# Kernel optimization log

Hardware: AMD Instinct MI355X
Metric: run time of the kernel (lower is better)

The kernel has to match this reference:

```python
import jax, jax.numpy as jnp
import numpy as np

NEG = -65504.0
D = 640


def _linear(x, W, b):
    return x @ W + b


def _qkv_attention(q, k, v, mask4):
    # q:[B,Lq,D] k,v:[B,Lk,D] mask4:[B,1,1,Lk] (True = masked)
    scores = jnp.einsum('bqd,bkd->bqk', q, k) / jnp.sqrt(jnp.asarray(q.shape[-1], q.dtype))
    scores = jnp.where(mask4[:, 0, :, :], NEG, scores)  # mask.squeeze(1) -> [B,1,Lk]
    p = jax.nn.softmax(scores, axis=-1)
    return jnp.einsum('bqk,bkd->bqd', p, v)


def _attflat(x, mask4, W1, b1, W2, b2, Wm, bm):
    # x:[B,N,D]; glimpses == 1
    att = _linear(jax.nn.relu(_linear(x, W1, b1)), W2, b2)  # [B,N,1]
    m = mask4[:, 0, 0, :, None]                              # [B,N,1]
    att = jnp.where(m, NEG, att)
    att = jax.nn.softmax(att, axis=1)
    pooled = jnp.sum(att * x, axis=1)                        # [B,D]
    return _linear(pooled, Wm, bm), att[..., 0]              # att.squeeze() -> [B,N]


def setup_inputs() -> dict:
    key = jax.random.key(0)
    ks = jax.random.split(key, 16)
    B, Ni, Nq = 64, 512, 128
    s = 0.02
    inp = {
        'i_batch': jax.random.normal(ks[0], (B, Ni, D), jnp.float32),
        'q_batch': jax.random.normal(ks[1], (B, Nq, D), jnp.float32),
        'i_mask': jax.random.bernoulli(ks[2], 0.3, (B, 1, 1, Ni)),
        'q_mask': jax.random.bernoulli(ks[3], 0.3, (B, 1, 1, Nq)),
        # l_flatten params (applied to image-side features)
        'lW1': jax.random.normal(ks[4], (D, 2 * D), jnp.float32) * s,
        'lb1': jnp.zeros((2 * D,), jnp.float32),
        'lW2': jax.random.normal(ks[5], (2 * D, 1), jnp.float32) * s,
        'lb2': jnp.zeros((1,), jnp.float32),
        'lWm': jax.random.normal(ks[6], (D, D), jnp.float32) * s,
        'lbm': jnp.zeros((D,), jnp.float32),
        # i_flatten params (applied to language-side features)
        'iW1': jax.random.normal(ks[7], (D, 2 * D), jnp.float32) * s,
        'ib1': jnp.zeros((2 * D,), jnp.float32),
        'iW2': jax.random.normal(ks[8], (2 * D, 1), jnp.float32) * s,
        'ib2': jnp.zeros((1,), jnp.float32),
        'iWm': jax.random.normal(ks[9], (D, D), jnp.float32) * s,
        'ibm': jnp.zeros((D,), jnp.float32),
    }
    return inp


def reference(i_batch, q_batch, i_mask, q_mask,
              lW1, lb1, lW2, lb2, lWm, lbm,
              iW1, ib1, iW2, ib2, iWm, ibm):
    # image attends over question tokens
    i_feat = _qkv_attention(i_batch, q_batch, q_batch, q_mask)   # [B,Ni,D]
    i_feat, i_weight = _attflat(i_feat, i_mask, lW1, lb1, lW2, lb2, lWm, lbm)
    # question attends over image regions
    l_feat = _qkv_attention(q_batch, i_batch, i_batch, i_mask)   # [B,Nq,D]
    l_feat, _ = _attflat(l_feat, q_mask, iW1, ib1, iW2, ib2, iWm, ibm)
    return (i_feat, l_feat, i_weight)
```

## Files before the change

kernel.cpp:

```cpp
#include <hip/hip_runtime.h>
#include <cstdint>

#define DEV __device__ __forceinline__

typedef __attribute__((ext_vector_type(8))) short bf16x8;
typedef __attribute__((ext_vector_type(4))) float f32x4;

static constexpr int B  = 64;
static constexpr int NI = 512;
static constexpr int NQ = 128;
static constexpr int D  = 640;
static constexpr int H  = 1280;
static constexpr float NEGV  = -65504.0f;
static constexpr float SCALE = 0.039528470752104745f;

DEV unsigned short f2bf(float f) {
  union { float f; uint32_t u; } c; c.f = f;
  uint32_t u = c.u;
  u += 0x7fffu + ((u >> 16) & 1u);
  return (unsigned short)(u >> 16);
}
DEV float bf2f(unsigned short h) {
  union { uint32_t u; float f; } c; c.u = ((uint32_t)h) << 16;
  return c.f;
}

DEV int xcd_swz(int bid, int nwg) {
  return (bid & 7) * (nwg >> 3) + (bid >> 3);
}

DEV void gll16(const void* g, void* l) {
  __builtin_amdgcn_global_load_lds(
      (const __attribute__((address_space(1))) void*)(uintptr_t)g,
      (__attribute__((address_space(3))) void*)(uint32_t)(uintptr_t)l,
      16, 0, 0);
}

DEV void stage64(const unsigned short* src, int ld, unsigned short* lds, int tid) {
  const int w = tid >> 6, lane = tid & 63;
#pragma unroll
  for (int i = 0; i < 4; ++i) {
    int c = w * 256 + i * 64 + lane;
    int r = c >> 3, ck = c & 7;
    int col8 = ((ck ^ (r & 7)) << 3);
    gll16(src + (long)r * ld + col8, (char*)lds + (size_t)c * 16);
  }
}

DEV bf16x8 frag(const unsigned short* ls, int row, int q) {
  return *(const bf16x8*)&ls[row * 64 + (((q ^ (row & 7))) << 3)];
}

template<int OUT_BF16>
__global__ __launch_bounds__(256, 4) void gemm_nt(
    const unsigned short* __restrict__ A, const unsigned short* __restrict__ Bt,
    void* __restrict__ C, int lda, int ldb, int ldc, int K,
    long sA, long sB, long sC, int gx, int gy)
{
  __shared__ __align__(16) unsigned short lsA[128 * 64];
  __shared__ __align__(16) unsigned short lsB[128 * 64];
  const int tid = threadIdx.x;
  const int w = tid >> 6, lane = tid & 63;
  const int wm = w >> 1, wn = w & 1;
  const int g = lane >> 4, r = lane & 15;
  const int wg = xcd_swz(blockIdx.x, gridDim.x);
  const int bz = wg / (gx * gy);
  const int r2 = wg - bz * gx * gy;
  const int by = r2 / gx;
  const int bx = r2 - by * gx;
  const long zb = bz;
  const unsigned short* Ab = A + zb * sA + (long)bx * 128 * lda;
  const unsigned short* Bb = Bt + zb * sB + (long)by * 128 * ldb;

  f32x4 acc[4][4] = {};
  for (int k0 = 0; k0 < K; k0 += 64) {
    stage64(Ab + k0, lda, lsA, tid);
    stage64(Bb + k0, ldb, lsB, tid);
    __syncthreads();
#pragma unroll
    for (int kk = 0; kk < 2; ++kk) {
      bf16x8 af[4], bfr[4];
#pragma unroll
      for (int mi = 0; mi < 4; ++mi) af[mi]  = frag(lsA, wm * 64 + mi * 16 + r, kk * 4 + g);
#pragma unroll
      for (int ni = 0; ni < 4; ++ni) bfr[ni] = frag(lsB, wn * 64 + ni * 16 + r, kk * 4 + g);
#pragma unroll
      for (int mi = 0; mi < 4; ++mi)
#pragma unroll
        for (int ni = 0; ni < 4; ++ni)
          acc[mi][ni] = __builtin_amdgcn_mfma_f32_16x16x32_bf16(af[mi], bfr[ni], acc[mi][ni], 0, 0, 0);
    }
    __syncthreads();
  }
  const int row0 = bx * 128 + wm * 64;
  const int col0 = by * 128 + wn * 64;
#pragma unroll
  for (int mi = 0; mi < 4; ++mi)
#pragma unroll
    for (int ni = 0; ni < 4; ++ni)
#pragma unroll
      for (int j = 0; j < 4; ++j) {
        int rr = row0 + mi * 16 + g * 4 + j;
        int cc = col0 + ni * 16 + r;
        float v = acc[mi][ni][j];
        if (OUT_BF16)
          ((unsigned short*)C)[zb * sC + (long)rr * ldc + cc] = f2bf(v);
        else
          ((float*)C)[zb * sC + (long)rr * ldc + cc] = v;
      }
}

__global__ __launch_bounds__(256, 2) void qksm_k(
    const unsigned short* __restrict__ A, const unsigned short* __restrict__ Bt,
    const int* __restrict__ mask, unsigned short* __restrict__ P)
{
  __shared__ __align__(16) float S[128 * 128];
  unsigned short* lsA = (unsigned short*)S;
  unsigned short* lsB = lsA + 128 * 64;
  const int tid = threadIdx.x;
  const int w = tid >> 6, lane = tid & 63;
  const int wm = w >> 1, wn = w & 1;
  const int g = lane >> 4, r = lane & 15;
  const int wg = xcd_swz(blockIdx.x, gridDim.x);
  const int mt = wg & 3, b = wg >> 2;
  const unsigned short* Ab = A + ((long)b * NI + (long)mt * 128) * D;
  const unsigned short* Bb = Bt + (long)b * NQ * D;

  f32x4 acc[4][4] = {};
  for (int k0 = 0; k0 < D; k0 += 64) {
    stage64(Ab + k0, D, lsA, tid);
    stage64(Bb + k0, D, lsB, tid);
    __syncthreads();
#pragma unroll
    for (int kk = 0; kk < 2; ++kk) {
      bf16x8 af[4], bfr[4];
#pragma unroll
      for (int mi = 0; mi < 4; ++mi) af[mi]  = frag(lsA, wm * 64 + mi * 16 + r, kk * 4 + g);
#pragma unroll
      for (int ni = 0; ni < 4; ++ni) bfr[ni] = frag(lsB, wn * 64 + ni * 16 + r, kk * 4 + g);
#pragma unroll
      for (int mi = 0; mi < 4; ++mi)
#pragma unroll
        for (int ni = 0; ni < 4; ++ni)
          acc[mi][ni] = __builtin_amdgcn_mfma_f32_16x16x32_bf16(af[mi], bfr[ni], acc[mi][ni], 0, 0, 0);
    }
    __syncthreads();
  }
#pragma unroll
  for (int mi = 0; mi < 4; ++mi)
#pragma unroll
    for (int ni = 0; ni < 4; ++ni)
#pragma unroll
      for (int j = 0; j < 4; ++j) {
        int rr = wm * 64 + mi * 16 + g * 4 + j;
        int cc = wn * 64 + ni * 16 + r;
        S[rr * 128 + (cc ^ ((rr & 7) << 2))] = acc[mi][ni][j] * SCALE;
      }
  __syncthreads();
  const int* mk = mask + (long)b * NQ;
  const int mk0 = mk[lane], mk1 = mk[lane + 64];
  for (int t = 0; t < 32; ++t) {
    const int rr = w * 32 + t;
    const int off = (rr & 7) << 2;
    float x0 = mk0 ? NEGV : S[rr * 128 + (lane ^ off)];
    float x1 = mk1 ? NEGV : S[rr * 128 + ((lane + 64) ^ off)];
    float mx = fmaxf(x0, x1);
#pragma unroll
    for (int s = 32; s >= 1; s >>= 1) mx = fmaxf(mx, __shfl_xor(mx, s));
    float e0 = __expf(x0 - mx), e1 = __expf(x1 - mx);
    float sum = e0 + e1;
#pragma unroll
    for (int s = 32; s >= 1; s >>= 1) sum += __shfl_xor(sum, s);
    const float inv = 1.f / sum;
    unsigned short* pr = P + ((long)b * NI + (long)mt * 128 + rr) * NQ;
    pr[lane] = f2bf(e0 * inv);
    pr[lane + 64] = f2bf(e1 * inv);
  }
}

__global__ __launch_bounds__(256, 4) void hatt_k(
    const unsigned short* __restrict__ A, const unsigned short* __restrict__ Bt,
    const float* __restrict__ b1, const float* __restrict__ W2,
    float* __restrict__ outlogit)
{
  constexpr int NH = H / 128;
  __shared__ __align__(16) unsigned short lsA[128 * 64];
  __shared__ __align__(16) unsigned short lsB[128 * 64];
  __shared__ float b1c[128], w2c[128];
  const int tid = threadIdx.x;
  const int w = tid >> 6, lane = tid & 63;
  const int wm = w >> 1, wn = w & 1;
  const int g = lane >> 4, r = lane & 15;
  const int wg = xcd_swz(blockIdx.x, gridDim.x);
  const int n0 = (wg % NH) * 128;
  const int m0 = (wg / NH) * 128;
  if (tid < 128) { b1c[tid] = b1[n0 + tid]; w2c[tid] = W2[n0 + tid]; }
  const unsigned short* Ab = A + (long)m0 * D;
  const unsigned short* Bb = Bt + (long)n0 * D;

  f32x4 acc[4][4] = {};
  for (int k0 = 0; k0 < D; k0 += 64) {
    stage64(Ab + k0, D, lsA, tid);
    stage64(Bb + k0, D, lsB, tid);
    __syncthreads();
#pragma unroll
    for (int kk = 0; kk < 2; ++kk) {
      bf16x8 af[4], bfr[4];
#pragma unroll
      for (int mi = 0; mi < 4; ++mi) af[mi]  = frag(lsA, wm * 64 + mi * 16 + r, kk * 4 + g);
#pragma unroll
      for (int ni = 0; ni < 4; ++ni) bfr[ni] = frag(lsB, wn * 64 + ni * 16 + r, kk * 4 + g);
#pragma unroll
      for (int mi = 0; mi < 4; ++mi)
#pragma unroll
        for (int ni = 0; ni < 4; ++ni)
          acc[mi][ni] = __builtin_amdgcn_mfma_f32_16x16x32_bf16(af[mi], bfr[ni], acc[mi][ni], 0, 0, 0);
    }
    __syncthreads();
  }
  float rs[4][4];
#pragma unroll
  for (int mi = 0; mi < 4; ++mi)
#pragma unroll
    for (int j = 0; j < 4; ++j) rs[mi][j] = 0.f;
#pragma unroll
  for (int mi = 0; mi < 4; ++mi)
#pragma unroll
    for (int ni = 0; ni < 4; ++ni)
#pragma unroll
      for (int j = 0; j < 4; ++j) {
        int cl = wn * 64 + ni * 16 + r;
        float h = acc[mi][ni][j] + b1c[cl];
        h = fmaxf(h, 0.f);
        rs[mi][j] += h * w2c[cl];
      }
#pragma unroll
  for (int mi = 0; mi < 4; ++mi)
#pragma unroll
    for (int j = 0; j < 4; ++j) {
      float v = rs[mi][j];
      v += __shfl_xor(v, 1); v += __shfl_xor(v, 2);
      v += __shfl_xor(v, 4); v += __shfl_xor(v, 8);
      if (r == 0) atomicAdd(&outlogit[m0 + wm * 64 + mi * 16 + g * 4 + j], v);
    }
}

template<int L>
__global__ void sm_scores(const float* __restrict__ S, const int* __restrict__ mask,
                          unsigned short* __restrict__ P, int M)
{
  constexpr int NV = L / 64;
  const int wid = threadIdx.x >> 6, lane = threadIdx.x & 63;
  const long row = (long)blockIdx.x * 4 + wid;
  const int b = (int)(row / M);
  const float* s = S + row * (long)L;
  const int* mk = mask + (long)b * L;
  float x[NV];
  float mx = -__builtin_inff();
#pragma unroll
  for (int i = 0; i < NV; ++i) {
    int idx = i * 64 + lane;
    float v = s[idx] * SCALE;
    x[i] = mk[idx] ? NEGV : v;
    mx = fmaxf(mx, x[i]);
  }
#pragma unroll
  for (int sft = 32; sft >= 1; sft >>= 1) mx = fmaxf(mx, __shfl_xor(mx, sft));
  float sum = 0.f;
#pragma unroll
  for (int i = 0; i < NV; ++i) { x[i] = __expf(x[i] - mx); sum += x[i]; }
#pragma unroll
  for (int sft = 32; sft >= 1; sft >>= 1) sum += __shfl_xor(sum, sft);
  const float inv = 1.f / sum;
  unsigned short* p = P + row * (long)L;
#pragma unroll
  for (int i = 0; i < NV; ++i) p[i * 64 + lane] = f2bf(x[i] * inv);
}

template<int L>
__global__ void sm_att(const float* __restrict__ logit, const int* __restrict__ mask,
                       const float* __restrict__ b2p, float* __restrict__ att,
                       float* __restrict__ iw)
{
  constexpr int PER = (L + 255) / 256;
  __shared__ float red[4];
  const int tid = threadIdx.x, b = blockIdx.x;
  const float b2v = b2p[0];
  float xs[PER];
  float mx = -__builtin_inff();
#pragma unroll
  for (int i = 0; i < PER; ++i) {
    int idx = tid + i * 256;
    if (idx < L) {
      float v = mask[(long)b * L + idx] ? NEGV : (logit[(long)b * L + idx] + b2v);
      xs[i] = v; mx = fmaxf(mx, v);
    } else xs[i] = -__builtin_inff();
  }
#pragma unroll
  for (int s = 32; s >= 1; s >>= 1) mx = fmaxf(mx, __shfl_xor(mx, s));
  if ((tid & 63) == 0) red[tid >> 6] = mx;
  __syncthreads();
  mx = fmaxf(fmaxf(red[0], red[1]), fmaxf(red[2], red[3]));
  __syncthreads();
  float sum = 0.f;
#pragma unroll
  for (int i = 0; i < PER; ++i) {
    int idx = tid + i * 256;
    if (idx < L) { xs[i] = __expf(xs[i] - mx); sum += xs[i]; }
  }
#pragma unroll
  for (int s = 32; s >= 1; s >>= 1) sum += __shfl_xor(sum, s);
  if ((tid & 63) == 0) red[tid >> 6] = sum;
  __syncthreads();
  sum = red[0] + red[1] + red[2] + red[3];
  const float inv = 1.f / sum;
#pragma unroll
  for (int i = 0; i < PER; ++i) {
    int idx = tid + i * 256;
    if (idx < L) {
      float a = xs[i] * inv;
      att[(long)b * L + idx] = a;
      if (iw) iw[(long)b * L + idx] = a;
    }
  }
}

template<int L>
__global__ void pooled_k(const float* __restrict__ att, const unsigned short* __restrict__ X,
                         float* __restrict__ out)
{
  __shared__ float a[L];
  __shared__ float2 part[8][64];
  const int b = blockIdx.x, tid = threadIdx.x;
  const int lane = tid & 63, grp = tid >> 6;
  const int d0 = blockIdx.y * 128 + lane * 2;
  for (int i = tid; i < L; i += 512) a[i] = att[(long)b * L + i];
  __syncthreads();
  const unsigned short* xb = X + (long)b * L * D + d0;
  float s0 = 0.f, s1 = 0.f;
  const int m0 = grp * (L / 8);
#pragma unroll 4
  for (int m = m0; m < m0 + L / 8; ++m) {
    ushort2 v = *(const ushort2*)&xb[(long)m * D];
    float av = a[m];
    s0 += av * bf2f(v.x); s1 += av * bf2f(v.y);
  }
  part[grp][lane] = make_float2(s0, s1);
  __syncthreads();
  if (tid < 64) {
    float r0 = 0.f, r1 = 0.f;
#pragma unroll
    for (int gi = 0; gi < 8; ++gi) { r0 += part[gi][tid].x; r1 += part[gi][tid].y; }
    *(float2*)&out[b * D + blockIdx.y * 128 + tid * 2] = make_float2(r0, r1);
  }
}

__global__ void final_k(const float* __restrict__ pooled, const float* __restrict__ W,
                        const float* __restrict__ bias, float* __restrict__ out)
{
  __shared__ float p[160];
  const int b = blockIdx.x, tid = threadIdx.x;
  const int nn = blockIdx.y * 128 + tid;
  const int k0 = blockIdx.z * 160;
  for (int i = tid; i < 160; i += 128) p[i] = pooled[b * D + k0 + i];
  __syncthreads();
  float acc = (blockIdx.z == 0) ? bias[nn] : 0.f;
  for (int k = 0; k < 160; ++k) acc += p[k] * W[(long)(k0 + k) * D + nn];
  atomicAdd(&out[b * D + nn], acc);
}

template<int WRITE_N>
__global__ void cast_t_k(const float* __restrict__ in, unsigned short* __restrict__ outN,
                         unsigned short* __restrict__ outT, int R, int C)
{
  __shared__ float t[64][65];
  const int tid = threadIdx.x;
  const int cg = tid & 15, rw = tid >> 4;
  const long base = (long)blockIdx.z * R * C;
  const int c0 = blockIdx.x * 64, r0 = blockIdx.y * 64;
#pragma unroll
  for (int p = 0; p < 4; ++p) {
    int row = p * 16 + rw;
    float4 v = *(const float4*)&in[base + (long)(r0 + row) * C + c0 + cg * 4];
    *(float4*)&t[row][cg * 4] = v;
    if (WRITE_N) {
      ushort4 o;
      o.x = f2bf(v.x); o.y = f2bf(v.y); o.z = f2bf(v.z); o.w = f2bf(v.w);
      *(ushort4*)&outN[base + (long)(r0 + row) * C + c0 + cg * 4] = o;
    }
  }
  __syncthreads();
#pragma unroll
  for (int p = 0; p < 4; ++p) {
    int ocol = p * 16 + rw;
    ushort4 o;
    o.x = f2bf(t[cg * 4 + 0][ocol]);
    o.y = f2bf(t[cg * 4 + 1][ocol]);
    o.z = f2bf(t[cg * 4 + 2][ocol]);
    o.w = f2bf(t[cg * 4 + 3][ocol]);
    *(ushort4*)&outT[base + (long)(c0 + ocol) * R + r0 + cg * 4] = o;
  }
}

extern "C" void kernel_launch(void* const* d_in, const int* in_sizes, int n_in,
                              void* d_out, int out_size, void* d_ws, size_t ws_size,
                              hipStream_t stream)
{
  (void)in_sizes; (void)n_in; (void)out_size; (void)ws_size;
  const float* i_batch = (const float*)d_in[0];
  const float* q_batch = (const float*)d_in[1];
  const int*   i_mask  = (const int*)d_in[2];
  const int*   q_mask  = (const int*)d_in[3];
  const float* lW1 = (const float*)d_in[4];
  const float* lb1 = (const float*)d_in[5];
  const float* lW2 = (const float*)d_in[6];
  const float* lb2 = (const float*)d_in[7];
  const float* lWm = (const float*)d_in[8];
  const float* lbm = (const float*)d_in[9];
  const float* iW1 = (const float*)d_in[10];
  const float* ib1 = (const float*)d_in[11];
  const float* iW2 = (const float*)d_in[12];
  const float* ib2 = (const float*)d_in[13];
  const float* iWm = (const float*)d_in[14];
  const float* ibm = (const float*)d_in[15];
  float* out_if = (float*)d_out;
  float* out_lf = out_if + B * D;
  float* out_iw = out_lf + B * D;

  char* wp = (char*)d_ws;
  size_t off = 0;
  auto alloc = [&](size_t bytes) { void* p = wp + off; off += (bytes + 255) & ~(size_t)255; return p; };
  unsigned short* i_bf   = (unsigned short*)alloc((size_t)B * NI * D * 2);
  unsigned short* i_bfT  = (unsigned short*)alloc((size_t)B * NI * D * 2);
  unsigned short* q_bf   = (unsigned short*)alloc((size_t)B * NQ * D * 2);
  unsigned short* q_bfT  = (unsigned short*)alloc((size_t)B * NQ * D * 2);
  unsigned short* x1_bf  = (unsigned short*)alloc((size_t)B * NI * D * 2);
  unsigned short* x2_bf  = (unsigned short*)alloc((size_t)B * NQ * D * 2);
  float*          scores = (float*)alloc((size_t)B * NQ * NI * 4);
  unsigned short* p_bf   = (unsigned short*)alloc((size_t)B * NI * NQ * 2);
  unsigned short* lW1t   = (unsigned short*)alloc((size_t)H * D * 2);
  unsigned short* iW1t   = (unsigned short*)alloc((size_t)H * D * 2);
  float* logit1  = (float*)alloc((size_t)B * NI * 4);
  float* att1    = (float*)alloc((size_t)B * NI * 4);
  float* logit2  = (float*)alloc((size_t)B * NQ * 4);
  float* att2    = (float*)alloc((size_t)B * NQ * 4);
  float* pooled1 = (float*)alloc((size_t)B * D * 4);
  float* pooled2 = (float*)alloc((size_t)B * D * 4);

  hipMemsetAsync(out_if, 0, (size_t)2 * B * D * 4, stream);
  hipMemsetAsync(logit1, 0, (size_t)(B * NI * 2 + B * NQ * 2) * 4, stream);

  cast_t_k<1><<<dim3(D / 64, NI / 64, B), 256, 0, stream>>>(i_batch, i_bf, i_bfT, NI, D);
  cast_t_k<1><<<dim3(D / 64, NQ / 64, B), 256, 0, stream>>>(q_batch, q_bf, q_bfT, NQ, D);
  cast_t_k<0><<<dim3(H / 64, D / 64, 1), 256, 0, stream>>>(lW1, nullptr, lW1t, D, H);
  cast_t_k<0><<<dim3(H / 64, D / 64, 1), 256, 0, stream>>>(iW1, nullptr, iW1t, D, H);

  qksm_k<<<dim3(4 * B), 256, 0, stream>>>(i_bf, q_bf, q_mask, p_bf);
  gemm_nt<1><<<dim3((NI / 128) * (D / 128) * B), 256, 0, stream>>>(
      p_bf, q_bfT, x1_bf, NQ, NQ, D, NQ, (long)NI * NQ, (long)D * NQ, (long)NI * D,
      NI / 128, D / 128);
  hatt_k<<<dim3((H / 128) * (B * NI / 128)), 256, 0, stream>>>(x1_bf, lW1t, lb1, lW2, logit1);
  sm_att<NI><<<dim3(B), 256, 0, stream>>>(logit1, i_mask, lb2, att1, out_iw);
  pooled_k<NI><<<dim3(B, D / 128), 512, 0, stream>>>(att1, x1_bf, pooled1);
  final_k<<<dim3(B, D / 128, 4), 128, 0, stream>>>(pooled1, lWm, lbm, out_if);

  gemm_nt<0><<<dim3((NQ / 128) * (NI / 128) * B), 256, 0, stream>>>(
      q_bf, i_bf, scores, D, D, NI, D, (long)NQ * D, (long)NI * D, (long)NQ * NI,
      NQ / 128, NI / 128);
  sm_scores<NI><<<dim3(B * NQ / 4), 256, 0, stream>>>(scores, i_mask, p_bf, NQ);
  gemm_nt<1><<<dim3((NQ / 128) * (D / 128) * B), 256, 0, stream>>>(
      p_bf, i_bfT, x2_bf, NI, NI, D, NI, (long)NQ * NI, (long)D * NI, (long)NQ * D,
      NQ / 128, D / 128);
  hatt_k<<<dim3((H / 128) * (B * NQ / 128)), 256, 0, stream>>>(x2_bf, iW1t, ib1, iW2, logit2);
  sm_att<NQ><<<dim3(B), 256, 0, stream>>>(logit2, q_mask, ib2, att2, nullptr);
  pooled_k<NQ><<<dim3(B, D / 128), 512, 0, stream>>>(att2, x2_bf, pooled2);
  final_k<<<dim3(B, D / 128, 4), 128, 0, stream>>>(pooled2, iWm, ibm, out_lf);
}
```

Baseline: 427.8 us.

## Fuse first attention into flash-style kernel, double-buffer GEMMs, fuse attflat tail

Replaces the first QK^T+softmax kernel and the following PV GEMM with one fused kernel. It keeps the probability tile in LDS and multiplies it by the transposed V in chunks, so the P matrix never goes to global memory. The generic GEMM and hatt kernels now double-buffer their LDS tiles, which overlaps the next tile's load with the current MFMA work but halves the occupancy bound. The softmax, pooling and final linear kernels are merged into a single per-batch tail kernel, which removes memsets and atomics but runs only 64 blocks with serial loops.

```diff
diff --git a/kernel.cpp b/kernel.cpp
--- a/kernel.cpp
+++ b/kernel.cpp
@@ -36,11 +36,12 @@
       16, 0, 0);
 }
 
-DEV void stage64(const unsigned short* src, int ld, unsigned short* lds, int tid) {
+template<int ROWS>
+DEV void stageT(const unsigned short* src, int ld, unsigned short* lds, int tid) {
   const int w = tid >> 6, lane = tid & 63;
 #pragma unroll
-  for (int i = 0; i < 4; ++i) {
-    int c = w * 256 + i * 64 + lane;
+  for (int i = 0; i < ROWS / 32; ++i) {
+    int c = w * (ROWS * 2) + i * 64 + lane;
     int r = c >> 3, ck = c & 7;
     int col8 = ((ck ^ (r & 7)) << 3);
     gll16(src + (long)r * ld + col8, (char*)lds + (size_t)c * 16);
@@ -48,17 +49,20 @@
 }
 
 DEV bf16x8 frag(const unsigned short* ls, int row, int q) {
-  return *(const bf16x8*)&ls[row * 64 + (((q ^ (row & 7))) << 3)];
+  return *(const bf16x8*)&ls[row * 64 + ((q ^ (row & 7)) << 3)];
+}
+DEV bf16x8 fragP(const unsigned short* P, int row, int q) {
+  return *(const bf16x8*)&P[row * 128 + ((q ^ (row & 7)) << 3)];
 }
 
 template<int OUT_BF16>
-__global__ __launch_bounds__(256, 4) void gemm_nt(
+__global__ __launch_bounds__(256, 2) void gemm_nt(
     const unsigned short* __restrict__ A, const unsigned short* __restrict__ Bt,
     void* __restrict__ C, int lda, int ldb, int ldc, int K,
     long sA, long sB, long sC, int gx, int gy)
 {
-  __shared__ __align__(16) unsigned short lsA[128 * 64];
-  __shared__ __align__(16) unsigned short lsB[128 * 64];
+  __shared__ __align__(16) unsigned short lsA[2][128 * 64];
+  __shared__ __align__(16) unsigned short lsB[2][128 * 64];
   const int tid = threadIdx.x;
   const int w = tid >> 6, lane = tid & 63;
   const int wm = w >> 1, wn = w & 1;
@@ -72,25 +76,31 @@
   const unsigned short* Ab = A + zb * sA + (long)bx * 128 * lda;
   const unsigned short* Bb = Bt + zb * sB + (long)by * 128 * ldb;
 
+  const int nt = K >> 6;
+  stageT<128>(Ab, lda, lsA[0], tid);
+  stageT<128>(Bb, ldb, lsB[0], tid);
   f32x4 acc[4][4] = {};
-  for (int k0 = 0; k0 < K; k0 += 64) {
-    stage64(Ab + k0, lda, lsA, tid);
-    stage64(Bb + k0, ldb, lsB, tid);
+  for (int t = 0; t < nt; ++t) {
     __syncthreads();
+    if (t + 1 < nt) {
+      stageT<128>(Ab + (t + 1) * 64, lda, lsA[(t + 1) & 1], tid);
+      stageT<128>(Bb + (t + 1) * 64, ldb, lsB[(t + 1) & 1], tid);
+    }
+    const unsigned short* la = lsA[t & 1];
+    const unsigned short* lb = lsB[t & 1];
 #pragma unroll
     for (int kk = 0; kk < 2; ++kk) {
       bf16x8 af[4], bfr[4];
 #pragma unroll
-      for (int mi = 0; mi < 4; ++mi) af[mi]  = frag(lsA, wm * 64 + mi * 16 + r, kk * 4 + g);
-#pragma unroll
-      for (int ni = 0; ni < 4; ++ni) bfr[ni] = frag(lsB, wn * 64 + ni * 16 + r, kk * 4 + g);
+      for (int mi = 0; mi < 4; ++mi) af[mi]  = frag(la, wm * 64 + mi * 16 + r, kk * 4 + g);
+#pragma unroll
+      for (int ni = 0; ni < 4; ++ni) bfr[ni] = frag(lb, wn * 64 + ni * 16 + r, kk * 4 + g);
 #pragma unroll
       for (int mi = 0; mi < 4; ++mi)
 #pragma unroll
         for (int ni = 0; ni < 4; ++ni)
           acc[mi][ni] = __builtin_amdgcn_mfma_f32_16x16x32_bf16(af[mi], bfr[ni], acc[mi][ni], 0, 0, 0);
     }
-    __syncthreads();
   }
   const int row0 = bx * 128 + wm * 64;
   const int col0 = by * 128 + wn * 64;
@@ -110,82 +120,175 @@
       }
 }
 
-__global__ __launch_bounds__(256, 2) void qksm_k(
-    const unsigned short* __restrict__ A, const unsigned short* __restrict__ Bt,
-    const int* __restrict__ mask, unsigned short* __restrict__ P)
-{
-  __shared__ __align__(16) float S[128 * 128];
-  unsigned short* lsA = (unsigned short*)S;
-  unsigned short* lsB = lsA + 128 * 64;
+__global__ __launch_bounds__(256, 2) void fattn1_k(
+    const unsigned short* __restrict__ Qm,
+    const unsigned short* __restrict__ Km,
+    const unsigned short* __restrict__ Vt,
+    const int* __restrict__ mask,
+    unsigned short* __restrict__ O)
+{
+  __shared__ __align__(16) unsigned short sh[64 * 64 + 128 * 64];
+  __shared__ __align__(16) unsigned short lsV[2][128 * 64];
+  __shared__ float red0[64][2], red1[64][2];
+  unsigned short* lsQ = sh;
+  unsigned short* lsK = sh + 64 * 64;
+  unsigned short* Pl  = sh;
   const int tid = threadIdx.x;
   const int w = tid >> 6, lane = tid & 63;
   const int wm = w >> 1, wn = w & 1;
   const int g = lane >> 4, r = lane & 15;
   const int wg = xcd_swz(blockIdx.x, gridDim.x);
-  const int mt = wg & 3, b = wg >> 2;
-  const unsigned short* Ab = A + ((long)b * NI + (long)mt * 128) * D;
-  const unsigned short* Bb = Bt + (long)b * NQ * D;
-
-  f32x4 acc[4][4] = {};
+  const int mt = wg & 7, b = wg >> 3;
+  const unsigned short* Qb = Qm + ((long)b * NI + (long)mt * 64) * D;
+  const unsigned short* Kb = Km + (long)b * NQ * D;
+  const unsigned short* Vb = Vt + (long)b * D * NQ;
+
+  int mki[4];
+#pragma unroll
+  for (int ni = 0; ni < 4; ++ni) mki[ni] = mask[b * NQ + wn * 64 + ni * 16 + r];
+
+  f32x4 acc[2][4] = {};
   for (int k0 = 0; k0 < D; k0 += 64) {
-    stage64(Ab + k0, D, lsA, tid);
-    stage64(Bb + k0, D, lsB, tid);
+    stageT<64>(Qb + k0, D, lsQ, tid);
+    stageT<128>(Kb + k0, D, lsK, tid);
     __syncthreads();
 #pragma unroll
     for (int kk = 0; kk < 2; ++kk) {
-      bf16x8 af[4], bfr[4];
-#pragma unroll
-      for (int mi = 0; mi < 4; ++mi) af[mi]  = frag(lsA, wm * 64 + mi * 16 + r, kk * 4 + g);
-#pragma unroll
-      for (int ni = 0; ni < 4; ++ni) bfr[ni] = frag(lsB, wn * 64 + ni * 16 + r, kk * 4 + g);
-#pragma unroll
-      for (int mi = 0; mi < 4; ++mi)
+      bf16x8 af[2], bfr[4];
+#pragma unroll
+      for (int mi = 0; mi < 2; ++mi) af[mi]  = frag(lsQ, wm * 32 + mi * 16 + r, kk * 4 + g);
+#pragma unroll
+      for (int ni = 0; ni < 4; ++ni) bfr[ni] = frag(lsK, wn * 64 + ni * 16 + r, kk * 4 + g);
+#pragma unroll
+      for (int mi = 0; mi < 2; ++mi)
 #pragma unroll
         for (int ni = 0; ni < 4; ++ni)
           acc[mi][ni] = __builtin_amdgcn_mfma_f32_16x16x32_bf16(af[mi], bfr[ni], acc[mi][ni], 0, 0, 0);
     }
     __syncthreads();
   }
-#pragma unroll
-  for (int mi = 0; mi < 4; ++mi)
+
+  float x[2][4][4], pm[2][4];
+#pragma unroll
+  for (int mi = 0; mi < 2; ++mi)
+#pragma unroll
+    for (int j = 0; j < 4; ++j) pm[mi][j] = -3.4e38f;
+#pragma unroll
+  for (int mi = 0; mi < 2; ++mi)
 #pragma unroll
     for (int ni = 0; ni < 4; ++ni)
 #pragma unroll
       for (int j = 0; j < 4; ++j) {
-        int rr = wm * 64 + mi * 16 + g * 4 + j;
-        int cc = wn * 64 + ni * 16 + r;
-        S[rr * 128 + (cc ^ ((rr & 7) << 2))] = acc[mi][ni][j] * SCALE;
+        float v = mki[ni] ? NEGV : acc[mi][ni][j] * SCALE;
+        x[mi][ni][j] = v;
+        pm[mi][j] = fmaxf(pm[mi][j], v);
       }
-  __syncthreads();
-  const int* mk = mask + (long)b * NQ;
-  const int mk0 = mk[lane], mk1 = mk[lane + 64];
-  for (int t = 0; t < 32; ++t) {
-    const int rr = w * 32 + t;
-    const int off = (rr & 7) << 2;
-    float x0 = mk0 ? NEGV : S[rr * 128 + (lane ^ off)];
-    float x1 = mk1 ? NEGV : S[rr * 128 + ((lane + 64) ^ off)];
-    float mx = fmaxf(x0, x1);
-#pragma unroll
-    for (int s = 32; s >= 1; s >>= 1) mx = fmaxf(mx, __shfl_xor(mx, s));
-    float e0 = __expf(x0 - mx), e1 = __expf(x1 - mx);
-    float sum = e0 + e1;
-#pragma unroll
-    for (int s = 32; s >= 1; s >>= 1) sum += __shfl_xor(sum, s);
-    const float inv = 1.f / sum;
-    unsigned short* pr = P + ((long)b * NI + (long)mt * 128 + rr) * NQ;
-    pr[lane] = f2bf(e0 * inv);
-    pr[lane + 64] = f2bf(e1 * inv);
-  }
-}
-
-__global__ __launch_bounds__(256, 4) void hatt_k(
+#pragma unroll
+  for (int s = 1; s < 16; s <<= 1)
+#pragma unroll
+    for (int mi = 0; mi < 2; ++mi)
+#pragma unroll
+      for (int j = 0; j < 4; ++j) pm[mi][j] = fmaxf(pm[mi][j], __shfl_xor(pm[mi][j], s));
+  if (r == 0) {
+#pragma unroll
+    for (int mi = 0; mi < 2; ++mi)
+#pragma unroll
+      for (int j = 0; j < 4; ++j) red0[wm * 32 + mi * 16 + g * 4 + j][wn] = pm[mi][j];
+  }
+  __syncthreads();
+  float mx[2][4], ps[2][4];
+#pragma unroll
+  for (int mi = 0; mi < 2; ++mi)
+#pragma unroll
+    for (int j = 0; j < 4; ++j) {
+      int rl = wm * 32 + mi * 16 + g * 4 + j;
+      mx[mi][j] = fmaxf(red0[rl][0], red0[rl][1]);
+      ps[mi][j] = 0.f;
+    }
+#pragma unroll
+  for (int mi = 0; mi < 2; ++mi)
+#pragma unroll
+    for (int ni = 0; ni < 4; ++ni)
+#pragma unroll
+      for (int j = 0; j < 4; ++j) {
+        float e = __expf(x[mi][ni][j] - mx[mi][j]);
+        x[mi][ni][j] = e;
+        ps[mi][j] += e;
+      }
+#pragma unroll
+  for (int s = 1; s < 16; s <<= 1)
+#pragma unroll
+    for (int mi = 0; mi < 2; ++mi)
+#pragma unroll
+      for (int j = 0; j < 4; ++j) ps[mi][j] += __shfl_xor(ps[mi][j], s);
+  if (r == 0) {
+#pragma unroll
+    for (int mi = 0; mi < 2; ++mi)
+#pragma unroll
+      for (int j = 0; j < 4; ++j) red1[wm * 32 + mi * 16 + g * 4 + j][wn] = ps[mi][j];
+  }
+  __syncthreads();
+#pragma unroll
+  for (int mi = 0; mi < 2; ++mi)
+#pragma unroll
+    for (int j = 0; j < 4; ++j) {
+      int rl = wm * 32 + mi * 16 + g * 4 + j;
+      float inv = 1.f / (red1[rl][0] + red1[rl][1]);
+#pragma unroll
+      for (int ni = 0; ni < 4; ++ni) {
+        int col = wn * 64 + ni * 16 + r;
+        Pl[rl * 128 + (((col >> 3) ^ (rl & 7)) << 3) + (col & 7)] = f2bf(x[mi][ni][j] * inv);
+      }
+    }
+  stageT<128>(Vb, 128, lsV[0], tid);
+  stageT<128>(Vb + 64, 128, lsV[1], tid);
+  __syncthreads();
+
+  for (int nc = 0; nc < 5; ++nc) {
+    if (nc > 0) __syncthreads();
+    f32x4 po[2][4] = {};
+#pragma unroll
+    for (int kk2 = 0; kk2 < 2; ++kk2)
+#pragma unroll
+      for (int kk = 0; kk < 2; ++kk) {
+        bf16x8 af[2], bfr[4];
+#pragma unroll
+        for (int mi = 0; mi < 2; ++mi) af[mi]  = fragP(Pl, wm * 32 + mi * 16 + r, kk2 * 8 + kk * 4 + g);
+#pragma unroll
+        for (int ni = 0; ni < 4; ++ni) bfr[ni] = frag(lsV[kk2], wn * 64 + ni * 16 + r, kk * 4 + g);
+#pragma unroll
+        for (int mi = 0; mi < 2; ++mi)
+#pragma unroll
+          for (int ni = 0; ni < 4; ++ni)
+            po[mi][ni] = __builtin_amdgcn_mfma_f32_16x16x32_bf16(af[mi], bfr[ni], po[mi][ni], 0, 0, 0);
+      }
+    __syncthreads();
+    if (nc < 4) {
+      const unsigned short* Vn = Vb + (long)(nc + 1) * 128 * 128;
+      stageT<128>(Vn, 128, lsV[0], tid);
+      stageT<128>(Vn + 64, 128, lsV[1], tid);
+    }
+#pragma unroll
+    for (int mi = 0; mi < 2; ++mi)
+#pragma unroll
+      for (int ni = 0; ni < 4; ++ni)
+#pragma unroll
+        for (int j = 0; j < 4; ++j) {
+          int rr = mt * 64 + wm * 32 + mi * 16 + g * 4 + j;
+          int cc = nc * 128 + wn * 64 + ni * 16 + r;
+          O[((long)b * NI + rr) * D + cc] = f2bf(po[mi][ni][j]);
+        }
+  }
+}
+
+__global__ __launch_bounds__(256, 2) void hatt_k(
     const unsigned short* __restrict__ A, const unsigned short* __restrict__ Bt,
     const float* __restrict__ b1, const float* __restrict__ W2,
     float* __restrict__ outlogit)
 {
   constexpr int NH = H / 128;
-  __shared__ __align__(16) unsigned short lsA[128 * 64];
-  __shared__ __align__(16) unsigned short lsB[128 * 64];
+  __shared__ __align__(16) unsigned short lsA[2][128 * 64];
+  __shared__ __align__(16) unsigned short lsB[2][128 * 64];
   __shared__ float b1c[128], w2c[128];
   const int tid = threadIdx.x;
   const int w = tid >> 6, lane = tid & 63;
@@ -198,25 +301,31 @@
   const unsigned short* Ab = A + (long)m0 * D;
   const unsigned short* Bb = Bt + (long)n0 * D;
 
+  constexpr int NT = D / 64;
+  stageT<128>(Ab, D, lsA[0], tid);
+  stageT<128>(Bb, D, lsB[0], tid);
   f32x4 acc[4][4] = {};
-  for (int k0 = 0; k0 < D; k0 += 64) {
-    stage64(Ab + k0, D, lsA, tid);
-    stage64(Bb + k0, D, lsB, tid);
+  for (int t = 0; t < NT; ++t) {
     __syncthreads();
+    if (t + 1 < NT) {
+      stageT<128>(Ab + (t + 1) * 64, D, lsA[(t + 1) & 1], tid);
+      stageT<128>(Bb + (t + 1) * 64, D, lsB[(t + 1) & 1], tid);
+    }
+    const unsigned short* la = lsA[t & 1];
+    const unsigned short* lb = lsB[t & 1];
 #pragma unroll
     for (int kk = 0; kk < 2; ++kk) {
       bf16x8 af[4], bfr[4];
 #pragma unroll
-      for (int mi = 0; mi < 4; ++mi) af[mi]  = frag(lsA, wm * 64 + mi * 16 + r, kk * 4 + g);
-#pragma unroll
-      for (int ni = 0; ni < 4; ++ni) bfr[ni] = frag(lsB, wn * 64 + ni * 16 + r, kk * 4 + g);
+      for (int mi = 0; mi < 4; ++mi) af[mi]  = frag(la, wm * 64 + mi * 16 + r, kk * 4 + g);
+#pragma unroll
+      for (int ni = 0; ni < 4; ++ni) bfr[ni] = frag(lb, wn * 64 + ni * 16 + r, kk * 4 + g);
 #pragma unroll
       for (int mi = 0; mi < 4; ++mi)
 #pragma unroll
         for (int ni = 0; ni < 4; ++ni)
           acc[mi][ni] = __builtin_amdgcn_mfma_f32_16x16x32_bf16(af[mi], bfr[ni], acc[mi][ni], 0, 0, 0);
     }
-    __syncthreads();
   }
   float rs[4][4];
 #pragma unroll
@@ -278,95 +387,49 @@
 }
 
 template<int L>
-__global__ void sm_att(const float* __restrict__ logit, const int* __restrict__ mask,
-                       const float* __restrict__ b2p, float* __restrict__ att,
-                       float* __restrict__ iw)
-{
-  constexpr int PER = (L + 255) / 256;
-  __shared__ float red[4];
+__global__ __launch_bounds__(640, 1) void tail_k(
+    const float* __restrict__ logit, const int* __restrict__ mask,
+    const float* __restrict__ b2p, const unsigned short* __restrict__ X,
+    const float* __restrict__ Wm, const float* __restrict__ bm,
+    float* __restrict__ outF, float* __restrict__ iw)
+{
+  __shared__ float att[L];
+  __shared__ float pool[D];
+  __shared__ float red[10];
   const int tid = threadIdx.x, b = blockIdx.x;
+  const int lane = tid & 63, wv = tid >> 6;
   const float b2v = b2p[0];
-  float xs[PER];
-  float mx = -__builtin_inff();
-#pragma unroll
-  for (int i = 0; i < PER; ++i) {
-    int idx = tid + i * 256;
-    if (idx < L) {
-      float v = mask[(long)b * L + idx] ? NEGV : (logit[(long)b * L + idx] + b2v);
-      xs[i] = v; mx = fmaxf(mx, v);
-    } else xs[i] = -__builtin_inff();
-  }
-#pragma unroll
-  for (int s = 32; s >= 1; s >>= 1) mx = fmaxf(mx, __shfl_xor(mx, s));
-  if ((tid & 63) == 0) red[tid >> 6] = mx;
-  __syncthreads();
-  mx = fmaxf(fmaxf(red[0], red[1]), fmaxf(red[2], red[3]));
-  __syncthreads();
-  float sum = 0.f;
-#pragma unroll
-  for (int i = 0; i < PER; ++i) {
-    int idx = tid + i * 256;
-    if (idx < L) { xs[i] = __expf(xs[i] - mx); sum += xs[i]; }
-  }
-#pragma unroll
-  for (int s = 32; s >= 1; s >>= 1) sum += __shfl_xor(sum, s);
-  if ((tid & 63) == 0) red[tid >> 6] = sum;
-  __syncthreads();
-  sum = red[0] + red[1] + red[2] + red[3];
-  const float inv = 1.f / sum;
-#pragma unroll
-  for (int i = 0; i < PER; ++i) {
-    int idx = tid + i * 256;
-    if (idx < L) {
-      float a = xs[i] * inv;
-      att[(long)b * L + idx] = a;
-      if (iw) iw[(long)b * L + idx] = a;
-    }
-  }
-}
-
-template<int L>
-__global__ void pooled_k(const float* __restrict__ att, const unsigned short* __restrict__ X,
-                         float* __restrict__ out)
-{
-  __shared__ float a[L];
-  __shared__ float2 part[8][64];
-  const int b = blockIdx.x, tid = threadIdx.x;
-  const int lane = tid & 63, grp = tid >> 6;
-  const int d0 = blockIdx.y * 128 + lane * 2;
-  for (int i = tid; i < L; i += 512) a[i] = att[(long)b * L + i];
-  __syncthreads();
-  const unsigned short* xb = X + (long)b * L * D + d0;
-  float s0 = 0.f, s1 = 0.f;
-  const int m0 = grp * (L / 8);
-#pragma unroll 4
-  for (int m = m0; m < m0 + L / 8; ++m) {
-    ushort2 v = *(const ushort2*)&xb[(long)m * D];
-    float av = a[m];
-    s0 += av * bf2f(v.x); s1 += av * bf2f(v.y);
-  }
-  part[grp][lane] = make_float2(s0, s1);
-  __syncthreads();
-  if (tid < 64) {
-    float r0 = 0.f, r1 = 0.f;
-#pragma unroll
-    for (int gi = 0; gi < 8; ++gi) { r0 += part[gi][tid].x; r1 += part[gi][tid].y; }
-    *(float2*)&out[b * D + blockIdx.y * 128 + tid * 2] = make_float2(r0, r1);
-  }
-}
-
-__global__ void final_k(const float* __restrict__ pooled, const float* __restrict__ W,
-                        const float* __restrict__ bias, float* __restrict__ out)
-{
-  __shared__ float p[160];
-  const int b = blockIdx.x, tid = threadIdx.x;
-  const int nn = blockIdx.y * 128 + tid;
-  const int k0 = blockIdx.z * 160;
-  for (int i = tid; i < 160; i += 128) p[i] = pooled[b * D + k0 + i];
-  __syncthreads();
-  float acc = (blockIdx.z == 0) ? bias[nn] : 0.f;
-  for (int k = 0; k < 160; ++k) acc += p[k] * W[(long)(k0 + k) * D + nn];
-  atomicAdd(&out[b * D + nn], acc);
+  float v = -__builtin_inff();
+  if (tid < L) v = mask[(long)b * L + tid] ? NEGV : (logit[(long)b * L + tid] + b2v);
+  float m = v;
+#pragma unroll
+  for (int s = 32; s >= 1; s >>= 1) m = fmaxf(m, __shfl_xor(m, s));
+  if (lane == 0) red[wv] = m;
+  __syncthreads();
+  float mx = red[0];
+#pragma unroll
+  for (int i = 1; i < 10; ++i) mx = fmaxf(mx, red[i]);
+  __syncthreads();
+  float e = (tid < L) ? __expf(v - mx) : 0.f;
+  float ssum = e;
+#pragma unroll
+  for (int s = 32; s >= 1; s >>= 1) ssum += __shfl_xor(ssum, s);
+  if (lane == 0) red[wv] = ssum;
+  __syncthreads();
+  float tot = 0.f;
+#pragma unroll
+  for (int i = 0; i < 10; ++i) tot += red[i];
+  const float a = e / tot;
+  if (tid < L) { att[tid] = a; if (iw) iw[(long)b * L + tid] = a; }
+  __syncthreads();
+  const unsigned short* Xb = X + (long)b * L * D + tid;
+  float s = 0.f;
+  for (int m2 = 0; m2 < L; ++m2) s += att[m2] * bf2f(Xb[(long)m2 * D]);
+  pool[tid] = s;
+  __syncthreads();
+  float o = bm[tid];
+  for (int k = 0; k < D; ++k) o += pool[k] * Wm[(long)k * D + tid];
+  outF[(long)b * D + tid] = o;
 }
 
 template<int WRITE_N>
@@ -437,32 +500,22 @@
   unsigned short* x1_bf  = (unsigned short*)alloc((size_t)B * NI * D * 2);
   unsigned short* x2_bf  = (unsigned short*)alloc((size_t)B * NQ * D * 2);
   float*          scores = (float*)alloc((size_t)B * NQ * NI * 4);
-  unsigned short* p_bf   = (unsigned short*)alloc((size_t)B * NI * NQ * 2);
+  unsigned short* p_bf   = (unsigned short*)alloc((size_t)B * NQ * NI * 2);
   unsigned short* lW1t   = (unsigned short*)alloc((size_t)H * D * 2);
   unsigned short* iW1t   = (unsigned short*)alloc((size_t)H * D * 2);
-  float* logit1  = (float*)alloc((size_t)B * NI * 4);
-  float* att1    = (float*)alloc((size_t)B * NI * 4);
-  float* logit2  = (float*)alloc((size_t)B * NQ * 4);
-  float* att2    = (float*)alloc((size_t)B * NQ * 4);
-  float* pooled1 = (float*)alloc((size_t)B * D * 4);
-  float* pooled2 = (float*)alloc((size_t)B * D * 4);
-
-  hipMemsetAsync(out_if, 0, (size_t)2 * B * D * 4, stream);
-  hipMemsetAsync(logit1, 0, (size_t)(B * NI * 2 + B * NQ * 2) * 4, stream);
+  float* logit1 = (float*)alloc((size_t)B * NI * 4);
+  float* logit2 = (float*)alloc((size_t)B * NQ * 4);
+
+  hipMemsetAsync(logit1, 0, (size_t)(B * NI + B * NQ) * 4, stream);
 
   cast_t_k<1><<<dim3(D / 64, NI / 64, B), 256, 0, stream>>>(i_batch, i_bf, i_bfT, NI, D);
   cast_t_k<1><<<dim3(D / 64, NQ / 64, B), 256, 0, stream>>>(q_batch, q_bf, q_bfT, NQ, D);
   cast_t_k<0><<<dim3(H / 64, D / 64, 1), 256, 0, stream>>>(lW1, nullptr, lW1t, D, H);
   cast_t_k<0><<<dim3(H / 64, D / 64, 1), 256, 0, stream>>>(iW1, nullptr, iW1t, D, H);
 
-  qksm_k<<<dim3(4 * B), 256, 0, stream>>>(i_bf, q_bf, q_mask, p_bf);
-  gemm_nt<1><<<dim3((NI / 128) * (D / 128) * B), 256, 0, stream>>>(
-      p_bf, q_bfT, x1_bf, NQ, NQ, D, NQ, (long)NI * NQ, (long)D * NQ, (long)NI * D,
-      NI / 128, D / 128);
+  fattn1_k<<<dim3(8 * B), 256, 0, stream>>>(i_bf, q_bf, q_bfT, q_mask, x1_bf);
   hatt_k<<<dim3((H / 128) * (B * NI / 128)), 256, 0, stream>>>(x1_bf, lW1t, lb1, lW2, logit1);
-  sm_att<NI><<<dim3(B), 256, 0, stream>>>(logit1, i_mask, lb2, att1, out_iw);
-  pooled_k<NI><<<dim3(B, D / 128), 512, 0, stream>>>(att1, x1_bf, pooled1);
-  final_k<<<dim3(B, D / 128, 4), 128, 0, stream>>>(pooled1, lWm, lbm, out_if);
+  tail_k<NI><<<dim3(B), 640, 0, stream>>>(logit1, i_mask, lb2, x1_bf, lWm, lbm, out_if, out_iw);
 
   gemm_nt<0><<<dim3((NQ / 128) * (NI / 128) * B), 256, 0, stream>>>(
       q_bf, i_bf, scores, D, D, NI, D, (long)NQ * D, (long)NI * D, (long)NQ * NI,
@@ -472,7 +525,5 @@
       p_bf, i_bfT, x2_bf, NI, NI, D, NI, (long)NQ * NI, (long)D * NI, (long)NQ * D,
       NQ / 128, D / 128);
   hatt_k<<<dim3((H / 128) * (B * NQ / 128)), 256, 0, stream>>>(x2_bf, iW1t, ib1, iW2, logit2);
-  sm_att<NQ><<<dim3(B), 256, 0, stream>>>(logit2, q_mask, ib2, att2, nullptr);
-  pooled_k<NQ><<<dim3(B, D / 128), 512, 0, stream>>>(att2, x2_bf, pooled2);
-  final_k<<<dim3(B, D / 128, 4), 128, 0, stream>>>(pooled2, iWm, ibm, out_lf);
-}
+  tail_k<NQ><<<dim3(B), 640, 0, stream>>>(logit2, q_mask, ib2, x2_bf, iWm, ibm, out_lf, nullptr);
+}
```

Result: no change. 427.3 us (-0.1%).
